# Optimization experiments

Measured on AMD Instinct MI355X. Metric: run time of the kernel, lower is better.

## Reference

```python
import jax, jax.numpy as jnp
import numpy as np

N_SHIFTS_TOTAL = 7  # n_shifts*2 + 1 with n_shifts=3
EPS = 1e-8


def setup_inputs() -> dict:
    key = jax.random.key(0)
    ks = jax.random.split(key, 10)
    B, DZ, L, D = 128, 1024, 4096, 256
    s = lambda k, shp, scale: (jax.random.normal(k, shp, dtype=jnp.float32) * scale)
    W_old = jax.random.uniform(ks[1], (B, L), dtype=jnp.float32)
    W_old = W_old / jnp.sum(W_old, axis=1, keepdims=True)  # valid address distribution
    return {
        "Z": jax.random.normal(ks[0], (B, DZ), dtype=jnp.float32),
        "W_old": W_old,
        "M": jax.random.normal(ks[2], (B, L, D), dtype=jnp.float32),
        # LecunNormal: stddev = 1/sqrt(fan_in)
        "key_W": s(ks[3], (DZ, D), DZ ** -0.5),
        "key_b": jnp.zeros((D,), jnp.float32),
        "shift_W": s(ks[4], (DZ, N_SHIFTS_TOTAL), DZ ** -0.5),
        "shift_b": jnp.zeros((N_SHIFTS_TOTAL,), jnp.float32),
        "beta_W": s(ks[5], (DZ, 1), DZ ** -0.5),
        "beta_b": jnp.zeros((1,), jnp.float32),
        "gate_W": s(ks[6], (DZ, 1), DZ ** -0.5),
        "gate_b": jnp.zeros((1,), jnp.float32),
        "gamma_W": s(ks[7], (DZ, 1), DZ ** -0.5),
        "gamma_b": jnp.zeros((1,), jnp.float32),
    }


def reference(Z, W_old, M, key_W, key_b, shift_W, shift_b,
              beta_W, beta_b, gate_W, gate_b, gamma_W, gamma_b):
    # Dense heads
    k = jnp.tanh(Z @ key_W + key_b)                              # [B, D]
    shift = jax.nn.softmax(Z @ shift_W + shift_b, axis=-1)      # [B, S]
    beta = jax.nn.softplus(Z @ beta_W + beta_b)                 # [B, 1]
    gate = jax.nn.sigmoid(Z @ gate_W + gate_b)                  # [B, 1]
    gamma = jax.nn.softplus(Z @ gamma_W + gamma_b) + 1.0        # [B, 1]

    # Content addressing: cosine similarity key vs each memory row
    k_norm = jnp.sqrt(jnp.sum(k * k, axis=1, keepdims=True))    # [B, 1]
    m_norm = jnp.sqrt(jnp.sum(M * M, axis=2))                   # [B, L]
    sim = jnp.einsum('bld,bd->bl', M, k) / (k_norm * m_norm + EPS)
    W = jax.nn.softmax(beta * sim, axis=1)                      # [B, L]

    # Interpolation with previous weights
    W = gate * W_old + (1.0 - gate) * W

    # Location addressing: circular convolution with shift kernel
    c = N_SHIFTS_TOTAL // 2
    rolled = jnp.stack([jnp.roll(W, n - c, axis=1)
                        for n in range(N_SHIFTS_TOTAL)], axis=1)  # [B, S, L]
    W = jnp.einsum('bsl,bs->bl', rolled, shift)

    # Sharpening
    W = jnp.power(W, gamma)
    return W / jnp.sum(W, axis=1, keepdims=True)
```

## Files before the change

### kernel.cpp

```cpp
#include <hip/hip_runtime.h>
#include <math.h>

constexpr int B  = 128;
constexpr int DZ = 1024;
constexpr int L  = 4096;
constexpr int D  = 256;
constexpr int S  = 7;
constexpr float EPS = 1e-8f;

static __device__ __forceinline__ float softplusf(float x) {
    return fmaxf(x, 0.0f) + log1pf(expf(-fabsf(x)));
}

__global__ __launch_bounds__(256) void heads_kernel(
    const float* __restrict__ Z,
    const float* __restrict__ key_W, const float* __restrict__ key_b,
    const float* __restrict__ shift_W, const float* __restrict__ shift_b,
    const float* __restrict__ beta_W, const float* __restrict__ beta_b,
    const float* __restrict__ gate_W, const float* __restrict__ gate_b,
    const float* __restrict__ gamma_W, const float* __restrict__ gamma_b,
    float* __restrict__ k_out, float* __restrict__ knorm_out,
    float* __restrict__ shift_out, float* __restrict__ beta_out,
    float* __restrict__ gate_out, float* __restrict__ gamma_out)
{
    const int b = blockIdx.x;
    const int t = threadIdx.x;

    __shared__ float zrow[DZ];
    __shared__ float red[256];

    for (int i = t; i < DZ; i += 256) zrow[i] = Z[b * DZ + i];
    __syncthreads();

    float a0 = 0.f, a1 = 0.f, a2 = 0.f, a3 = 0.f;
    for (int z = 0; z < DZ; z += 4) {
        a0 = fmaf(zrow[z + 0], key_W[(z + 0) * D + t], a0);
        a1 = fmaf(zrow[z + 1], key_W[(z + 1) * D + t], a1);
        a2 = fmaf(zrow[z + 2], key_W[(z + 2) * D + t], a2);
        a3 = fmaf(zrow[z + 3], key_W[(z + 3) * D + t], a3);
    }
    float kv = tanhf((a0 + a1) + (a2 + a3) + key_b[t]);
    k_out[b * D + t] = kv;

    red[t] = kv * kv;
    __syncthreads();
    for (int st = 128; st > 0; st >>= 1) {
        if (t < st) red[t] += red[t + st];
        __syncthreads();
    }
    if (t == 0) knorm_out[b] = sqrtf(red[0]);

    float part[10];
#pragma unroll
    for (int j = 0; j < 10; ++j) part[j] = 0.f;
    for (int z = t; z < DZ; z += 256) {
        const float zv = zrow[z];
#pragma unroll
        for (int j = 0; j < S; ++j) part[j] = fmaf(zv, shift_W[z * S + j], part[j]);
        part[7] = fmaf(zv, beta_W[z],  part[7]);
        part[8] = fmaf(zv, gate_W[z],  part[8]);
        part[9] = fmaf(zv, gamma_W[z], part[9]);
    }
#pragma unroll
    for (int j = 0; j < 10; ++j) {
        __syncthreads();
        red[t] = part[j];
        __syncthreads();
        for (int st = 128; st > 0; st >>= 1) {
            if (t < st) red[t] += red[t + st];
            __syncthreads();
        }
        if (t == 0) part[j] = red[0];
    }

    if (t == 0) {
        float logits[S];
        float mx = -1e30f;
#pragma unroll
        for (int j = 0; j < S; ++j) {
            logits[j] = part[j] + shift_b[j];
            mx = fmaxf(mx, logits[j]);
        }
        float sum = 0.f;
#pragma unroll
        for (int j = 0; j < S; ++j) {
            logits[j] = expf(logits[j] - mx);
            sum += logits[j];
        }
        const float inv = 1.f / sum;
#pragma unroll
        for (int j = 0; j < S; ++j) shift_out[b * S + j] = logits[j] * inv;

        beta_out[b]  = softplusf(part[7] + beta_b[0]);
        gate_out[b]  = 1.f / (1.f + expf(-(part[8] + gate_b[0])));
        gamma_out[b] = softplusf(part[9] + gamma_b[0]) + 1.0f;
    }
}

constexpr int ROWS_PER_BLOCK = 16;

__global__ __launch_bounds__(256) void sim_kernel(
    const float* __restrict__ M,
    const float* __restrict__ k,
    const float* __restrict__ knorm,
    const float* __restrict__ beta,
    float* __restrict__ s_out)
{
    const int blk   = blockIdx.x;
    const int b     = blk / (L / ROWS_PER_BLOCK);
    const int chunk = blk % (L / ROWS_PER_BLOCK);
    const int wave  = threadIdx.x >> 6;
    const int lane  = threadIdx.x & 63;

    __shared__ float4 k_lds[64];
    if (threadIdx.x < 64) k_lds[threadIdx.x] = ((const float4*)(k + b * D))[threadIdx.x];
    __syncthreads();

    const float4 kv = k_lds[lane];
    const float  kn = knorm[b];
    const float  bt = beta[b];

    const int l0 = chunk * ROWS_PER_BLOCK + wave * 4;
    const float4* Mrow0 = (const float4*)(M + ((size_t)b * L + l0) * D);

    float4 mv[4];
#pragma unroll
    for (int r = 0; r < 4; ++r) mv[r] = Mrow0[(size_t)r * (D / 4) + lane];

#pragma unroll
    for (int r = 0; r < 4; ++r) {
        float dot = mv[r].x * kv.x + mv[r].y * kv.y + mv[r].z * kv.z + mv[r].w * kv.w;
        float msq = mv[r].x * mv[r].x + mv[r].y * mv[r].y + mv[r].z * mv[r].z + mv[r].w * mv[r].w;
#pragma unroll
        for (int off = 32; off > 0; off >>= 1) {
            dot += __shfl_xor(dot, off);
            msq += __shfl_xor(msq, off);
        }
        if (lane == 0) {
            const float sim = dot / (kn * sqrtf(msq) + EPS);
            s_out[(size_t)b * L + l0 + r] = bt * sim;
        }
    }
}

__global__ __launch_bounds__(256) void finish_kernel(
    const float* __restrict__ s,
    const float* __restrict__ W_old,
    const float* __restrict__ shiftv,
    const float* __restrict__ gate,
    const float* __restrict__ gamma,
    float* __restrict__ out)
{
    const int b = blockIdx.x;
    const int t = threadIdx.x;

    __shared__ float w[L];
    __shared__ float red[256];
    __shared__ float sh[S];

    float vals[16];
    float mx = -1e30f;
#pragma unroll
    for (int i = 0; i < 16; ++i) {
        vals[i] = s[(size_t)b * L + t + i * 256];
        mx = fmaxf(mx, vals[i]);
    }
    red[t] = mx;
    __syncthreads();
    for (int st = 128; st > 0; st >>= 1) {
        if (t < st) red[t] = fmaxf(red[t], red[t + st]);
        __syncthreads();
    }
    mx = red[0];
    __syncthreads();

    float sum = 0.f;
#pragma unroll
    for (int i = 0; i < 16; ++i) {
        vals[i] = expf(vals[i] - mx);
        sum += vals[i];
    }
    red[t] = sum;
    __syncthreads();
    for (int st = 128; st > 0; st >>= 1) {
        if (t < st) red[t] += red[t + st];
        __syncthreads();
    }
    const float invsum = 1.f / red[0];
    __syncthreads();

    const float g = gate[b];
#pragma unroll
    for (int i = 0; i < 16; ++i) {
        const int l = t + i * 256;
        w[l] = fmaf(g, W_old[(size_t)b * L + l], (1.f - g) * (vals[i] * invsum));
    }
    if (t < S) sh[t] = shiftv[b * S + t];
    __syncthreads();

    const float gm = gamma[b];
    float pv[16];
    float psum = 0.f;
#pragma unroll
    for (int i = 0; i < 16; ++i) {
        const int l = t + i * 256;
        float acc = 0.f;
#pragma unroll
        for (int n = 0; n < S; ++n)
            acc = fmaf(sh[n], w[(l - n + 3 + L) & (L - 1)], acc);
        const float p = powf(acc, gm);
        pv[i] = p;
        psum += p;
    }
    red[t] = psum;
    __syncthreads();
    for (int st = 128; st > 0; st >>= 1) {
        if (t < st) red[t] += red[t + st];
        __syncthreads();
    }
    const float invp = 1.f / red[0];
#pragma unroll
    for (int i = 0; i < 16; ++i)
        out[(size_t)b * L + t + i * 256] = pv[i] * invp;
}

extern "C" void kernel_launch(void* const* d_in, const int* in_sizes, int n_in,
                              void* d_out, int out_size, void* d_ws, size_t ws_size,
                              hipStream_t stream)
{
    const float* Z       = (const float*)d_in[0];
    const float* W_old   = (const float*)d_in[1];
    const float* M       = (const float*)d_in[2];
    const float* key_W   = (const float*)d_in[3];
    const float* key_b   = (const float*)d_in[4];
    const float* shift_W = (const float*)d_in[5];
    const float* shift_b = (const float*)d_in[6];
    const float* beta_W  = (const float*)d_in[7];
    const float* beta_b  = (const float*)d_in[8];
    const float* gate_W  = (const float*)d_in[9];
    const float* gate_b  = (const float*)d_in[10];
    const float* gamma_W = (const float*)d_in[11];
    const float* gamma_b = (const float*)d_in[12];
    float* out = (float*)d_out;

    float* ws     = (float*)d_ws;
    float* k      = ws;
    float* knorm  = k + B * D;
    float* shiftv = knorm + B;
    float* betav  = shiftv + B * S;
    float* gatev  = betav + B;
    float* gammav = gatev + B;
    float* s      = gammav + B;

    heads_kernel<<<B, 256, 0, stream>>>(Z, key_W, key_b, shift_W, shift_b,
                                        beta_W, beta_b, gate_W, gate_b,
                                        gamma_W, gamma_b,
                                        k, knorm, shiftv, betav, gatev, gammav);

    sim_kernel<<<B * (L / ROWS_PER_BLOCK), 256, 0, stream>>>(M, k, knorm, betav, s);

    finish_kernel<<<B, 256, 0, stream>>>(s, W_old, shiftv, gatev, gammav, out);
}
```

Baseline: 750.2 us.

## Restructure all three kernels: batched head reductions, multi-row sim waves, wave-shuffle finish

The heads kernel now reduces all eleven partial sums (including the key norm) in a single shared-memory tree instead of eleven sequential ones. The sim kernel processes 64 rows per block, with each 16-lane group handling one row, and double-buffers the M loads across four row-passes, which cuts the shuffle depth and the block count. The finish kernel uses 1024 threads with wave-shuffle reductions and swaps in fast exp/log2 intrinsics in place of powf/expf. The intent is to stream M more efficiently and remove reduction and synchronization overhead, at some precision risk from the fast math intrinsics.

Result: no change. 738.6 us (-1.5%).

```diff
diff --git a/kernel.cpp b/kernel.cpp
--- a/kernel.cpp
+++ b/kernel.cpp
@@ -26,33 +26,27 @@
     const int b = blockIdx.x;
     const int t = threadIdx.x;
 
+    constexpr int RSTRIDE = 257;
     __shared__ float zrow[DZ];
-    __shared__ float red[256];
+    __shared__ float red[11 * RSTRIDE];
 
     for (int i = t; i < DZ; i += 256) zrow[i] = Z[b * DZ + i];
     __syncthreads();
 
-    float a0 = 0.f, a1 = 0.f, a2 = 0.f, a3 = 0.f;
-    for (int z = 0; z < DZ; z += 4) {
-        a0 = fmaf(zrow[z + 0], key_W[(z + 0) * D + t], a0);
-        a1 = fmaf(zrow[z + 1], key_W[(z + 1) * D + t], a1);
-        a2 = fmaf(zrow[z + 2], key_W[(z + 2) * D + t], a2);
-        a3 = fmaf(zrow[z + 3], key_W[(z + 3) * D + t], a3);
-    }
-    float kv = tanhf((a0 + a1) + (a2 + a3) + key_b[t]);
+    float acc = 0.f;
+    for (int zb = 0; zb < DZ; zb += 16) {
+        float p = 0.f;
+#pragma unroll
+        for (int u = 0; u < 16; ++u)
+            p = fmaf(zrow[zb + u], key_W[(zb + u) * D + t], p);
+        acc += p;
+    }
+    const float kv = tanhf(acc + key_b[t]);
     k_out[b * D + t] = kv;
 
-    red[t] = kv * kv;
-    __syncthreads();
-    for (int st = 128; st > 0; st >>= 1) {
-        if (t < st) red[t] += red[t + st];
-        __syncthreads();
-    }
-    if (t == 0) knorm_out[b] = sqrtf(red[0]);
-
-    float part[10];
-#pragma unroll
-    for (int j = 0; j < 10; ++j) part[j] = 0.f;
+    float part[11];
+#pragma unroll
+    for (int j = 0; j < 11; ++j) part[j] = 0.f;
     for (int z = t; z < DZ; z += 256) {
         const float zv = zrow[z];
 #pragma unroll
@@ -61,16 +55,18 @@
         part[8] = fmaf(zv, gate_W[z],  part[8]);
         part[9] = fmaf(zv, gamma_W[z], part[9]);
     }
-#pragma unroll
-    for (int j = 0; j < 10; ++j) {
+    part[10] = kv * kv;
+
+#pragma unroll
+    for (int j = 0; j < 11; ++j) red[j * RSTRIDE + t] = part[j];
+    __syncthreads();
+    for (int st = 128; st > 0; st >>= 1) {
+        if (t < st) {
+#pragma unroll
+            for (int j = 0; j < 11; ++j)
+                red[j * RSTRIDE + t] += red[j * RSTRIDE + t + st];
+        }
         __syncthreads();
-        red[t] = part[j];
-        __syncthreads();
-        for (int st = 128; st > 0; st >>= 1) {
-            if (t < st) red[t] += red[t + st];
-            __syncthreads();
-        }
-        if (t == 0) part[j] = red[0];
     }
 
     if (t == 0) {
@@ -78,7 +74,7 @@
         float mx = -1e30f;
 #pragma unroll
         for (int j = 0; j < S; ++j) {
-            logits[j] = part[j] + shift_b[j];
+            logits[j] = red[j * RSTRIDE] + shift_b[j];
             mx = fmaxf(mx, logits[j]);
         }
         float sum = 0.f;
@@ -91,13 +87,12 @@
 #pragma unroll
         for (int j = 0; j < S; ++j) shift_out[b * S + j] = logits[j] * inv;
 
-        beta_out[b]  = softplusf(part[7] + beta_b[0]);
-        gate_out[b]  = 1.f / (1.f + expf(-(part[8] + gate_b[0])));
-        gamma_out[b] = softplusf(part[9] + gamma_b[0]) + 1.0f;
-    }
-}
-
-constexpr int ROWS_PER_BLOCK = 16;
+        beta_out[b]  = softplusf(red[7 * RSTRIDE] + beta_b[0]);
+        gate_out[b]  = 1.f / (1.f + expf(-(red[8 * RSTRIDE] + gate_b[0])));
+        gamma_out[b] = softplusf(red[9 * RSTRIDE] + gamma_b[0]) + 1.0f;
+        knorm_out[b] = sqrtf(red[10 * RSTRIDE]);
+    }
+}
 
 __global__ __launch_bounds__(256) void sim_kernel(
     const float* __restrict__ M,
@@ -107,43 +102,58 @@
     float* __restrict__ s_out)
 {
     const int blk   = blockIdx.x;
-    const int b     = blk / (L / ROWS_PER_BLOCK);
-    const int chunk = blk % (L / ROWS_PER_BLOCK);
+    const int b     = blk >> 6;
+    const int chunk = blk & 63;
     const int wave  = threadIdx.x >> 6;
     const int lane  = threadIdx.x & 63;
-
-    __shared__ float4 k_lds[64];
-    if (threadIdx.x < 64) k_lds[threadIdx.x] = ((const float4*)(k + b * D))[threadIdx.x];
-    __syncthreads();
-
-    const float4 kv = k_lds[lane];
-    const float  kn = knorm[b];
-    const float  bt = beta[b];
-
-    const int l0 = chunk * ROWS_PER_BLOCK + wave * 4;
-    const float4* Mrow0 = (const float4*)(M + ((size_t)b * L + l0) * D);
-
-    float4 mv[4];
-#pragma unroll
-    for (int r = 0; r < 4; ++r) mv[r] = Mrow0[(size_t)r * (D / 4) + lane];
-
-#pragma unroll
-    for (int r = 0; r < 4; ++r) {
-        float dot = mv[r].x * kv.x + mv[r].y * kv.y + mv[r].z * kv.z + mv[r].w * kv.w;
-        float msq = mv[r].x * mv[r].x + mv[r].y * mv[r].y + mv[r].z * mv[r].z + mv[r].w * mv[r].w;
-#pragma unroll
-        for (int off = 32; off > 0; off >>= 1) {
+    const int sub   = lane >> 4;
+    const int l16   = lane & 15;
+
+    const float4* kp = (const float4*)(k + b * D);
+    float4 kv[4];
+#pragma unroll
+    for (int j = 0; j < 4; ++j) kv[j] = kp[l16 + 16 * j];
+
+    const float kn = knorm[b];
+    const float bt = beta[b];
+
+    const int l0 = chunk * 64 + wave * 16;
+    const float4* Mp = (const float4*)(M + ((size_t)b * L + l0) * D);
+
+    float4 mv[2][4];
+#pragma unroll
+    for (int j = 0; j < 4; ++j)
+        mv[0][j] = Mp[(size_t)sub * 64 + l16 + 16 * j];
+
+#pragma unroll
+    for (int p = 0; p < 4; ++p) {
+        if (p < 3) {
+#pragma unroll
+            for (int j = 0; j < 4; ++j)
+                mv[(p + 1) & 1][j] = Mp[(size_t)((p + 1) * 4 + sub) * 64 + l16 + 16 * j];
+        }
+        const float4* m = mv[p & 1];
+        float dot = 0.f, msq = 0.f;
+#pragma unroll
+        for (int j = 0; j < 4; ++j) {
+            dot = fmaf(m[j].x, kv[j].x, dot); msq = fmaf(m[j].x, m[j].x, msq);
+            dot = fmaf(m[j].y, kv[j].y, dot); msq = fmaf(m[j].y, m[j].y, msq);
+            dot = fmaf(m[j].z, kv[j].z, dot); msq = fmaf(m[j].z, m[j].z, msq);
+            dot = fmaf(m[j].w, kv[j].w, dot); msq = fmaf(m[j].w, m[j].w, msq);
+        }
+#pragma unroll
+        for (int off = 8; off > 0; off >>= 1) {
             dot += __shfl_xor(dot, off);
             msq += __shfl_xor(msq, off);
         }
-        if (lane == 0) {
+        if (l16 == 0) {
             const float sim = dot / (kn * sqrtf(msq) + EPS);
-            s_out[(size_t)b * L + l0 + r] = bt * sim;
-        }
-    }
-}
-
-__global__ __launch_bounds__(256) void finish_kernel(
+            s_out[(size_t)b * L + l0 + p * 4 + sub] = bt * sim;
+        }
+    }
+}
+
+__global__ __launch_bounds__(1024) void finish_kernel(
     const float* __restrict__ s,
     const float* __restrict__ W_old,
     const float* __restrict__ shiftv,
@@ -151,77 +161,81 @@
     const float* __restrict__ gamma,
     float* __restrict__ out)
 {
-    const int b = blockIdx.x;
-    const int t = threadIdx.x;
+    const int b    = blockIdx.x;
+    const int t    = threadIdx.x;
+    const int wid  = t >> 6;
+    const int lane = t & 63;
 
     __shared__ float w[L];
-    __shared__ float red[256];
+    __shared__ float partial[16];
     __shared__ float sh[S];
 
-    float vals[16];
+    float vals[4];
     float mx = -1e30f;
 #pragma unroll
-    for (int i = 0; i < 16; ++i) {
-        vals[i] = s[(size_t)b * L + t + i * 256];
+    for (int i = 0; i < 4; ++i) {
+        vals[i] = s[(size_t)b * L + t + i * 1024];
         mx = fmaxf(mx, vals[i]);
     }
-    red[t] = mx;
-    __syncthreads();
-    for (int st = 128; st > 0; st >>= 1) {
-        if (t < st) red[t] = fmaxf(red[t], red[t + st]);
-        __syncthreads();
-    }
-    mx = red[0];
+#pragma unroll
+    for (int off = 32; off > 0; off >>= 1) mx = fmaxf(mx, __shfl_xor(mx, off));
+    if (lane == 0) partial[wid] = mx;
+    __syncthreads();
+    float m = partial[0];
+#pragma unroll
+    for (int j = 1; j < 16; ++j) m = fmaxf(m, partial[j]);
     __syncthreads();
 
     float sum = 0.f;
 #pragma unroll
-    for (int i = 0; i < 16; ++i) {
-        vals[i] = expf(vals[i] - mx);
+    for (int i = 0; i < 4; ++i) {
+        vals[i] = __expf(vals[i] - m);
         sum += vals[i];
     }
-    red[t] = sum;
-    __syncthreads();
-    for (int st = 128; st > 0; st >>= 1) {
-        if (t < st) red[t] += red[t + st];
-        __syncthreads();
-    }
-    const float invsum = 1.f / red[0];
+#pragma unroll
+    for (int off = 32; off > 0; off >>= 1) sum += __shfl_xor(sum, off);
+    if (lane == 0) partial[wid] = sum;
+    __syncthreads();
+    float tot = 0.f;
+#pragma unroll
+    for (int j = 0; j < 16; ++j) tot += partial[j];
+    const float invsum = 1.f / tot;
     __syncthreads();
 
     const float g = gate[b];
 #pragma unroll
-    for (int i = 0; i < 16; ++i) {
-        const int l = t + i * 256;
+    for (int i = 0; i < 4; ++i) {
+        const int l = t + i * 1024;
         w[l] = fmaf(g, W_old[(size_t)b * L + l], (1.f - g) * (vals[i] * invsum));
     }
     if (t < S) sh[t] = shiftv[b * S + t];
     __syncthreads();
 
     const float gm = gamma[b];
-    float pv[16];
+    float pv[4];
     float psum = 0.f;
 #pragma unroll
-    for (int i = 0; i < 16; ++i) {
-        const int l = t + i * 256;
+    for (int i = 0; i < 4; ++i) {
+        const int l = t + i * 1024;
         float acc = 0.f;
 #pragma unroll
         for (int n = 0; n < S; ++n)
-            acc = fmaf(sh[n], w[(l - n + 3 + L) & (L - 1)], acc);
-        const float p = powf(acc, gm);
+            acc = fmaf(sh[n], w[(l - n + 3) & (L - 1)], acc);
+        const float p = exp2f(gm * log2f(acc));
         pv[i] = p;
         psum += p;
     }
-    red[t] = psum;
-    __syncthreads();
-    for (int st = 128; st > 0; st >>= 1) {
-        if (t < st) red[t] += red[t + st];
-        __syncthreads();
-    }
-    const float invp = 1.f / red[0];
-#pragma unroll
-    for (int i = 0; i < 16; ++i)
-        out[(size_t)b * L + t + i * 256] = pv[i] * invp;
+#pragma unroll
+    for (int off = 32; off > 0; off >>= 1) psum += __shfl_xor(psum, off);
+    if (lane == 0) partial[wid] = psum;
+    __syncthreads();
+    float ptot = 0.f;
+#pragma unroll
+    for (int j = 0; j < 16; ++j) ptot += partial[j];
+    const float invp = 1.f / ptot;
+#pragma unroll
+    for (int i = 0; i < 4; ++i)
+        out[(size_t)b * L + t + i * 1024] = pv[i] * invp;
 }
 
 extern "C" void kernel_launch(void* const* d_in, const int* in_sizes, int n_in,
@@ -257,7 +271,7 @@
                                         gamma_W, gamma_b,
                                         k, knorm, shiftv, betav, gatev, gammav);
 
-    sim_kernel<<<B * (L / ROWS_PER_BLOCK), 256, 0, stream>>>(M, k, knorm, betav, s);
-
-    finish_kernel<<<B, 256, 0, stream>>>(s, W_old, shiftv, gatev, gammav, out);
-}
+    sim_kernel<<<B * (L / 64), 256, 0, stream>>>(M, k, knorm, betav, s);
+
+    finish_kernel<<<B, 1024, 0, stream>>>(s, W_old, shiftv, gatev, gammav, out);
+}
```
